# Performance work log

Measured on AMD Instinct MI355X. Metric: run time of the kernel, lower is better.

Reference implementation:

```python
import jax, jax.numpy as jnp
import numpy as np

IN_COUNT, OUT_COUNT, NUM_BASIS = 512, 512, 8
X_MIN, X_MAX, GAMMA_SCALE = 0.0, 1.0, 3.0
BATCH = 8192


def setup_inputs() -> dict:
    key = jax.random.key(0)
    k_x, k_c = jax.random.split(key)
    x = jax.random.uniform(k_x, (BATCH, IN_COUNT), dtype=jnp.float32)
    coeffs = 0.01 * jax.random.normal(k_c, (OUT_COUNT, IN_COUNT, NUM_BASIS), dtype=jnp.float32)
    centers_1d = jnp.linspace(X_MIN, X_MAX, NUM_BASIS, dtype=jnp.float32)
    centers = jnp.tile(centers_1d[None, :], (IN_COUNT, 1))  # (in, basis)
    delta = (X_MAX - X_MIN) / (NUM_BASIS - 1)
    gamma = GAMMA_SCALE / delta
    slopes = jnp.full((IN_COUNT, NUM_BASIS), gamma, dtype=jnp.float32)
    return {"x": x, "coeffs": coeffs, "centers": centers, "slopes": slopes}


def reference(x, coeffs, centers, slopes):
    # s_im(x) = 0.5 * (1 + tanh(gamma_im * (x_bi - c_im)))  -> (batch, in, basis)
    basis = 0.5 * (1.0 + jnp.tanh(slopes[None, :, :] * (x[:, :, None] - centers[None, :, :])))
    # y_bj = sum_{i,m} a_jim * s_bim : fused double reduction (GEMM-shaped)
    y = jnp.einsum('bim,jim->bj', basis, coeffs)
    return y
```

## Files before the change

kernel.cpp:

```cpp
#include <hip/hip_runtime.h>

#define BATCH 8192
#define INC   512
#define OUTC  512
#define NB    8
#define KDIM  (INC * NB)

#define BM 64
#define BN 128
#define BK 64
#define NKT (KDIM / BK)
#define LDA 72
#define THREADS 256

typedef __attribute__((ext_vector_type(8))) short bf16x8;
typedef __attribute__((ext_vector_type(4))) float f32x4;
typedef __attribute__((ext_vector_type(4))) int   i32x4;

static __device__ __forceinline__ unsigned int pk2(float lo, float hi) {
    return __builtin_amdgcn_perm(__builtin_bit_cast(unsigned int, hi),
                                 __builtin_bit_cast(unsigned int, lo),
                                 0x07060302u);
}

static __device__ __forceinline__ i32x4 pk8(float4 a, float4 b) {
    return (i32x4){(int)pk2(a.x, a.y), (int)pk2(a.z, a.w),
                   (int)pk2(b.x, b.y), (int)pk2(b.z, b.w)};
}

__global__ __launch_bounds__(256)
void w_prepass(const float* __restrict__ W, unsigned short* __restrict__ Wb) {
    const int base = (blockIdx.x * 256 + threadIdx.x) * 8;
    const float4 a = *(const float4*)(W + base);
    const float4 b = *(const float4*)(W + base + 4);
    const float v[8] = {a.x, a.y, a.z, a.w, b.x, b.y, b.z, b.w};
    unsigned int r[8];
#pragma unroll
    for (int i = 0; i < 8; ++i) {
        unsigned int t = __builtin_bit_cast(unsigned int, v[i]);
        t += 0x7FFFu + ((t >> 16) & 1u);
        r[i] = t >> 16;
    }
    i32x4 out = {(int)(r[0] | (r[1] << 16)), (int)(r[2] | (r[3] << 16)),
                 (int)(r[4] | (r[5] << 16)), (int)(r[6] | (r[7] << 16))};
    *(i32x4*)(Wb + base) = out;
}

template <bool DMA>
__global__ __launch_bounds__(THREADS, 2)
void tanh_basis_fused_gemm(const float* __restrict__ X,
                           const void*  __restrict__ Wsrc,
                           const float* __restrict__ CEN,
                           const float* __restrict__ SLP,
                           float* __restrict__ Y)
{
    __shared__ short As[BM][LDA];
    __shared__ short Bs[BN * BK];

    const int tid  = threadIdx.x;
    const int lane = tid & 63;
    const int wave = tid >> 6;
    const int wm   = wave & 1;
    const int wn   = wave >> 1;

    const int b0 = blockIdx.x * BM;
    const int j0 = blockIdx.y * BN;

    const float L2E = 1.4426950408889634f;
    const float g2  = 2.0f * SLP[0] * L2E;
    const float pc  = -g2;
    const float q0  = g2 * CEN[0];
    const float R   = __builtin_amdgcn_exp2f(g2 * (CEN[1] - CEN[0]));

    const int arow = tid >> 2;
    const int acol = (tid & 3) * 2;
    const float* xp = X + (size_t)(b0 + arow) * INC + acol;

    f32x4 acc[2][4];
#pragma unroll
    for (int i = 0; i < 2; ++i)
#pragma unroll
        for (int j = 0; j < 4; ++j)
            acc[i][j] = (f32x4){0.f, 0.f, 0.f, 0.f};

    const short* const arp = &As[wm * 32 + (lane & 15)][(lane >> 4) * 8];
    const short* const brp = &Bs[(wn * 64 + (lane & 15)) * BK + (lane >> 4) * 8];

    float2 xv = *(const float2*)xp;

    for (int kt = 0; kt < NKT; ++kt) {
        if constexpr (DMA) {
            const unsigned short* Wb = (const unsigned short*)Wsrc;
#pragma unroll
            for (int q = 0; q < 4; ++q) {
                const int cc = wave * 4 + q;
                const unsigned short* gp = Wb
                    + (size_t)(j0 + cc * 8 + (lane >> 3)) * KDIM
                    + kt * BK + (lane & 7) * 8;
                __builtin_amdgcn_global_load_lds(
                    (const __attribute__((address_space(1))) void*)gp,
                    (__attribute__((address_space(3))) void*)(Bs + cc * 512),
                    16, 0, 0);
            }
        } else {
            const float* Wf = (const float*)Wsrc;
            const int brow = tid >> 1;
            const int bkh  = tid & 1;
            const float* wp = Wf + (size_t)(j0 + brow) * KDIM + kt * BK + bkh * 32;
            float4 cv[8];
#pragma unroll
            for (int q = 0; q < 8; ++q) cv[q] = ((const float4*)wp)[q];
            i32x4* bw = (i32x4*)(Bs + brow * BK + bkh * 32);
            bw[0] = pk8(cv[0], cv[1]);
            bw[1] = pk8(cv[2], cv[3]);
            bw[2] = pk8(cv[4], cv[5]);
            bw[3] = pk8(cv[6], cv[7]);
        }

        const int ktn = (kt + 1 < NKT) ? (kt + 1) : (NKT - 1);
        const float2 xn = *(const float2*)(xp + ktn * NB);

        {
            float t0 = fmaf(pc, xv.x, q0);
            float e  = __builtin_amdgcn_exp2f(t0);
            float s[NB];
#pragma unroll
            for (int m = 0; m < NB; ++m) {
                s[m] = __builtin_amdgcn_rcpf(1.0f + e);
                e *= R;
            }
            *(i32x4*)(&As[arow][acol * 8]) =
                (i32x4){(int)pk2(s[0], s[1]), (int)pk2(s[2], s[3]),
                        (int)pk2(s[4], s[5]), (int)pk2(s[6], s[7])};

            t0 = fmaf(pc, xv.y, q0);
            e  = __builtin_amdgcn_exp2f(t0);
#pragma unroll
            for (int m = 0; m < NB; ++m) {
                s[m] = __builtin_amdgcn_rcpf(1.0f + e);
                e *= R;
            }
            *(i32x4*)(&As[arow][(acol + 1) * 8]) =
                (i32x4){(int)pk2(s[0], s[1]), (int)pk2(s[2], s[3]),
                        (int)pk2(s[4], s[5]), (int)pk2(s[6], s[7])};
        }

        __syncthreads();

#pragma unroll
        for (int ks = 0; ks < 2; ++ks) {
            bf16x8 af[2], bfr[4];
#pragma unroll
            for (int mf = 0; mf < 2; ++mf)
                af[mf] = *(const bf16x8*)(arp + mf * 16 * LDA + ks * 32);
#pragma unroll
            for (int nf = 0; nf < 4; ++nf)
                bfr[nf] = *(const bf16x8*)(brp + nf * 16 * BK + ks * 32);
#pragma unroll
            for (int mf = 0; mf < 2; ++mf)
#pragma unroll
                for (int nf = 0; nf < 4; ++nf)
                    acc[mf][nf] = __builtin_amdgcn_mfma_f32_16x16x32_bf16(
                        af[mf], bfr[nf], acc[mf][nf], 0, 0, 0);
        }

        __syncthreads();

        xv = xn;
    }

    const int lm = (lane >> 4) * 4;
    const int ln = lane & 15;
    const int rowb = b0 + wm * 32 + lm;
    const int colb = j0 + wn * 64 + ln;
#pragma unroll
    for (int mf = 0; mf < 2; ++mf)
#pragma unroll
        for (int nf = 0; nf < 4; ++nf)
#pragma unroll
            for (int r = 0; r < 4; ++r)
                Y[(size_t)(rowb + mf * 16 + r) * OUTC + (colb + nf * 16)] = acc[mf][nf][r];
}

extern "C" void kernel_launch(void* const* d_in, const int* in_sizes, int n_in,
                              void* d_out, int out_size, void* d_ws, size_t ws_size,
                              hipStream_t stream) {
    const float* X   = (const float*)d_in[0];
    const float* W   = (const float*)d_in[1];
    const float* CEN = (const float*)d_in[2];
    const float* SLP = (const float*)d_in[3];
    float* Y = (float*)d_out;

    static_assert(BATCH % BM == 0 && OUTC % BN == 0 && KDIM % BK == 0, "tiling");
    dim3 grid(BATCH / BM, OUTC / BN);

    const size_t WB_BYTES = (size_t)OUTC * KDIM * sizeof(unsigned short);
    if (ws_size >= WB_BYTES) {
        w_prepass<<<dim3((OUTC * KDIM) / (8 * 256)), dim3(256), 0, stream>>>(
            W, (unsigned short*)d_ws);
        tanh_basis_fused_gemm<true><<<grid, dim3(THREADS), 0, stream>>>(
            X, d_ws, CEN, SLP, Y);
    } else {
        tanh_basis_fused_gemm<false><<<grid, dim3(THREADS), 0, stream>>>(
            X, (const void*)W, CEN, SLP, Y);
    }
}
```

Before: 135.1 us.

## Split-K fused GEMM with register-computed basis, double-buffered swizzled B, transposed X

Restructures the fused kernel. It uses 4-way split-K with atomicAdd into a zeroed output, larger 128x128 tiles with 2 waves each holding a 64x128 accumulator, and double-buffered XOR-swizzled LDS for the bf16 weights. The tanh-basis A fragments are now built directly in registers instead of being staged through LDS. A new prepass transposes X so each lane's x loads coalesce across the batch. Together these aim to cut LDS traffic and syncs and to overlap weight staging with compute. The cost is extra prepass and memset launches, float atomics that make summation order nondeterministic, and heavy register pressure from the 32 accumulators.

```diff
diff --git a/kernel.cpp b/kernel.cpp
--- a/kernel.cpp
+++ b/kernel.cpp
@@ -5,13 +5,13 @@
 #define OUTC  512
 #define NB    8
 #define KDIM  (INC * NB)
-
-#define BM 64
-#define BN 128
-#define BK 64
-#define NKT (KDIM / BK)
-#define LDA 72
-#define THREADS 256
+#define SPLITK 4
+#define KQ    (KDIM / SPLITK)
+#define BK    64
+#define NKT   (KQ / BK)
+#define BM    128
+#define BN    128
+#define THREADS 128
 
 typedef __attribute__((ext_vector_type(8))) short bf16x8;
 typedef __attribute__((ext_vector_type(4))) float f32x4;
@@ -21,11 +21,6 @@
     return __builtin_amdgcn_perm(__builtin_bit_cast(unsigned int, hi),
                                  __builtin_bit_cast(unsigned int, lo),
                                  0x07060302u);
-}
-
-static __device__ __forceinline__ i32x4 pk8(float4 a, float4 b) {
-    return (i32x4){(int)pk2(a.x, a.y), (int)pk2(a.z, a.w),
-                   (int)pk2(b.x, b.y), (int)pk2(b.z, b.w)};
 }
 
 __global__ __launch_bounds__(256)
@@ -41,30 +36,52 @@
         t += 0x7FFFu + ((t >> 16) & 1u);
         r[i] = t >> 16;
     }
-    i32x4 out = {(int)(r[0] | (r[1] << 16)), (int)(r[2] | (r[3] << 16)),
-                 (int)(r[4] | (r[5] << 16)), (int)(r[6] | (r[7] << 16))};
-    *(i32x4*)(Wb + base) = out;
-}
-
-template <bool DMA>
+    *(i32x4*)(Wb + base) = (i32x4){(int)(r[0] | (r[1] << 16)), (int)(r[2] | (r[3] << 16)),
+                                   (int)(r[4] | (r[5] << 16)), (int)(r[6] | (r[7] << 16))};
+}
+
+__global__ __launch_bounds__(256)
+void xt_prepass(const float* __restrict__ X, float* __restrict__ XT) {
+    __shared__ float t[64][65];
+    const int bx = blockIdx.x * 64;
+    const int iy = blockIdx.y * 64;
+    const int lx = threadIdx.x & 63;
+    const int ly = threadIdx.x >> 6;
+#pragma unroll
+    for (int r = 0; r < 16; ++r) {
+        const int row = ly * 16 + r;
+        t[row][lx] = X[(size_t)(bx + row) * INC + iy + lx];
+    }
+    __syncthreads();
+#pragma unroll
+    for (int r = 0; r < 16; ++r) {
+        const int row = ly * 16 + r;
+        XT[(size_t)(iy + row) * BATCH + bx + lx] = t[lx][row];
+    }
+}
+
+template <bool DMA, bool XTP>
 __global__ __launch_bounds__(THREADS, 2)
-void tanh_basis_fused_gemm(const float* __restrict__ X,
-                           const void*  __restrict__ Wsrc,
-                           const float* __restrict__ CEN,
-                           const float* __restrict__ SLP,
-                           float* __restrict__ Y)
+void fused_gemm(const float* __restrict__ X,
+                const void*  __restrict__ Wsrc,
+                const float* __restrict__ XT,
+                const float* __restrict__ CEN,
+                const float* __restrict__ SLP,
+                float* __restrict__ Y)
 {
-    __shared__ short As[BM][LDA];
-    __shared__ short Bs[BN * BK];
+    __shared__ short Bs[2][BN * BK];
 
     const int tid  = threadIdx.x;
     const int lane = tid & 63;
     const int wave = tid >> 6;
-    const int wm   = wave & 1;
-    const int wn   = wave >> 1;
+    const int l15  = lane & 15;
+    const int h    = lane >> 4;
+    const int low3 = l15 & 7;
 
     const int b0 = blockIdx.x * BM;
     const int j0 = blockIdx.y * BN;
+    const int kz = blockIdx.z;
+    const int i00 = kz * (KQ / NB);
 
     const float L2E = 1.4426950408889634f;
     const float g2  = 2.0f * SLP[0] * L2E;
@@ -72,114 +89,126 @@
     const float q0  = g2 * CEN[0];
     const float R   = __builtin_amdgcn_exp2f(g2 * (CEN[1] - CEN[0]));
 
-    const int arow = tid >> 2;
-    const int acol = (tid & 3) * 2;
-    const float* xp = X + (size_t)(b0 + arow) * INC + acol;
-
-    f32x4 acc[2][4];
-#pragma unroll
-    for (int i = 0; i < 2; ++i)
-#pragma unroll
-        for (int j = 0; j < 4; ++j)
+    const short* const brp0 = &Bs[0][l15 * 64 + ((0 + h) ^ low3) * 8];
+    const short* const brp1 = &Bs[0][l15 * 64 + ((4 + h) ^ low3) * 8];
+
+    const int dma_r  = lane >> 3;
+    const int dma_kb = (lane & 7) ^ dma_r;
+
+    const int mrow = b0 + wave * 64 + l15;
+
+    f32x4 acc[4][8];
+#pragma unroll
+    for (int i = 0; i < 4; ++i)
+#pragma unroll
+        for (int j = 0; j < 8; ++j)
             acc[i][j] = (f32x4){0.f, 0.f, 0.f, 0.f};
 
-    const short* const arp = &As[wm * 32 + (lane & 15)][(lane >> 4) * 8];
-    const short* const brp = &Bs[(wn * 64 + (lane & 15)) * BK + (lane >> 4) * 8];
-
-    float2 xv = *(const float2*)xp;
+    float xv[8], xn[8];
+
+#define LOADX(kt, dst)                                                         \
+    {                                                                          \
+        _Pragma("unroll")                                                      \
+        for (int ks = 0; ks < 2; ++ks) {                                       \
+            const int ii = i00 + (kt) * 8 + ks * 4 + h;                        \
+            _Pragma("unroll")                                                  \
+            for (int mf = 0; mf < 4; ++mf) {                                   \
+                const int bb = mrow + mf * 16;                                 \
+                (dst)[ks * 4 + mf] = XTP ? XT[(size_t)ii * BATCH + bb]         \
+                                         : X[(size_t)bb * INC + ii];           \
+            }                                                                  \
+        }                                                                      \
+    }
+
+#define STAGEB(kt, buf)                                                        \
+    {                                                                          \
+        const int kg = kz * KQ + (kt) * BK;                                    \
+        if constexpr (DMA) {                                                   \
+            const unsigned short* Wb = (const unsigned short*)Wsrc;            \
+            _Pragma("unroll")                                                  \
+            for (int q = 0; q < 8; ++q) {                                      \
+                const int cc = wave * 8 + q;                                   \
+                const unsigned short* gp = Wb                                  \
+                    + (size_t)(j0 + cc * 8 + dma_r) * KDIM + kg + dma_kb * 8;  \
+                __builtin_amdgcn_global_load_lds(                              \
+                    (const __attribute__((address_space(1))) void*)gp,         \
+                    (__attribute__((address_space(3))) void*)(&Bs[buf][cc * 512]), \
+                    16, 0, 0);                                                 \
+            }                                                                  \
+        } else {                                                               \
+            const float* Wf = (const float*)Wsrc;                              \
+            const int row = tid;                                               \
+            const float* wp = Wf + (size_t)(j0 + row) * KDIM + kg;             \
+            _Pragma("unroll")                                                  \
+            for (int kb = 0; kb < 8; ++kb) {                                   \
+                const float4 c0 = ((const float4*)wp)[2 * kb];                 \
+                const float4 c1 = ((const float4*)wp)[2 * kb + 1];             \
+                *(i32x4*)(&Bs[buf][row * 64 + ((kb ^ (row & 7)) * 8)]) =       \
+                    (i32x4){(int)pk2(c0.x, c0.y), (int)pk2(c0.z, c0.w),        \
+                            (int)pk2(c1.x, c1.y), (int)pk2(c1.z, c1.w)};       \
+            }                                                                  \
+        }                                                                      \
+    }
+
+    LOADX(0, xv);
+    STAGEB(0, 0);
 
     for (int kt = 0; kt < NKT; ++kt) {
-        if constexpr (DMA) {
-            const unsigned short* Wb = (const unsigned short*)Wsrc;
-#pragma unroll
-            for (int q = 0; q < 4; ++q) {
-                const int cc = wave * 4 + q;
-                const unsigned short* gp = Wb
-                    + (size_t)(j0 + cc * 8 + (lane >> 3)) * KDIM
-                    + kt * BK + (lane & 7) * 8;
-                __builtin_amdgcn_global_load_lds(
-                    (const __attribute__((address_space(1))) void*)gp,
-                    (__attribute__((address_space(3))) void*)(Bs + cc * 512),
-                    16, 0, 0);
+        const int cur = kt & 1;
+
+        __syncthreads();
+
+        if (kt + 1 < NKT) STAGEB(kt + 1, 1 - cur);
+        const int ktn = (kt + 1 < NKT) ? (kt + 1) : (NKT - 1);
+        LOADX(ktn, xn);
+
+#pragma unroll
+        for (int ks = 0; ks < 2; ++ks) {
+            const short* brp = (ks ? brp1 : brp0) + cur * (BN * BK);
+            bf16x8 bfr[8];
+#pragma unroll
+            for (int nf = 0; nf < 8; ++nf)
+                bfr[nf] = *(const bf16x8*)(brp + nf * 1024);
+
+            bf16x8 af[4];
+#pragma unroll
+            for (int mf = 0; mf < 4; ++mf) {
+                float e = __builtin_amdgcn_exp2f(fmaf(pc, xv[ks * 4 + mf], q0));
+                float s[NB];
+#pragma unroll
+                for (int m = 0; m < NB; ++m) {
+                    s[m] = __builtin_amdgcn_rcpf(1.0f + e);
+                    e *= R;
+                }
+                af[mf] = __builtin_bit_cast(bf16x8,
+                    (i32x4){(int)pk2(s[0], s[1]), (int)pk2(s[2], s[3]),
+                            (int)pk2(s[4], s[5]), (int)pk2(s[6], s[7])});
             }
-        } else {
-            const float* Wf = (const float*)Wsrc;
-            const int brow = tid >> 1;
-            const int bkh  = tid & 1;
-            const float* wp = Wf + (size_t)(j0 + brow) * KDIM + kt * BK + bkh * 32;
-            float4 cv[8];
-#pragma unroll
-            for (int q = 0; q < 8; ++q) cv[q] = ((const float4*)wp)[q];
-            i32x4* bw = (i32x4*)(Bs + brow * BK + bkh * 32);
-            bw[0] = pk8(cv[0], cv[1]);
-            bw[1] = pk8(cv[2], cv[3]);
-            bw[2] = pk8(cv[4], cv[5]);
-            bw[3] = pk8(cv[6], cv[7]);
-        }
-
-        const int ktn = (kt + 1 < NKT) ? (kt + 1) : (NKT - 1);
-        const float2 xn = *(const float2*)(xp + ktn * NB);
-
-        {
-            float t0 = fmaf(pc, xv.x, q0);
-            float e  = __builtin_amdgcn_exp2f(t0);
-            float s[NB];
-#pragma unroll
-            for (int m = 0; m < NB; ++m) {
-                s[m] = __builtin_amdgcn_rcpf(1.0f + e);
-                e *= R;
-            }
-            *(i32x4*)(&As[arow][acol * 8]) =
-                (i32x4){(int)pk2(s[0], s[1]), (int)pk2(s[2], s[3]),
-                        (int)pk2(s[4], s[5]), (int)pk2(s[6], s[7])};
-
-            t0 = fmaf(pc, xv.y, q0);
-            e  = __builtin_amdgcn_exp2f(t0);
-#pragma unroll
-            for (int m = 0; m < NB; ++m) {
-                s[m] = __builtin_amdgcn_rcpf(1.0f + e);
-                e *= R;
-            }
-            *(i32x4*)(&As[arow][(acol + 1) * 8]) =
-                (i32x4){(int)pk2(s[0], s[1]), (int)pk2(s[2], s[3]),
-                        (int)pk2(s[4], s[5]), (int)pk2(s[6], s[7])};
-        }
-
-        __syncthreads();
-
-#pragma unroll
-        for (int ks = 0; ks < 2; ++ks) {
-            bf16x8 af[2], bfr[4];
-#pragma unroll
-            for (int mf = 0; mf < 2; ++mf)
-                af[mf] = *(const bf16x8*)(arp + mf * 16 * LDA + ks * 32);
-#pragma unroll
-            for (int nf = 0; nf < 4; ++nf)
-                bfr[nf] = *(const bf16x8*)(brp + nf * 16 * BK + ks * 32);
-#pragma unroll
-            for (int mf = 0; mf < 2; ++mf)
-#pragma unroll
-                for (int nf = 0; nf < 4; ++nf)
+
+#pragma unroll
+            for (int mf = 0; mf < 4; ++mf)
+#pragma unroll
+                for (int nf = 0; nf < 8; ++nf)
                     acc[mf][nf] = __builtin_amdgcn_mfma_f32_16x16x32_bf16(
                         af[mf], bfr[nf], acc[mf][nf], 0, 0, 0);
         }
 
-        __syncthreads();
-
-        xv = xn;
-    }
-
-    const int lm = (lane >> 4) * 4;
-    const int ln = lane & 15;
-    const int rowb = b0 + wm * 32 + lm;
-    const int colb = j0 + wn * 64 + ln;
-#pragma unroll
-    for (int mf = 0; mf < 2; ++mf)
-#pragma unroll
-        for (int nf = 0; nf < 4; ++nf)
+#pragma unroll
+        for (int q = 0; q < 8; ++q) xv[q] = xn[q];
+    }
+
+    const int rowb = b0 + wave * 64 + h * 4;
+    const int colb = j0 + l15;
+#pragma unroll
+    for (int mf = 0; mf < 4; ++mf)
+#pragma unroll
+        for (int nf = 0; nf < 8; ++nf)
 #pragma unroll
             for (int r = 0; r < 4; ++r)
-                Y[(size_t)(rowb + mf * 16 + r) * OUTC + (colb + nf * 16)] = acc[mf][nf][r];
+                atomicAdd(&Y[(size_t)(rowb + mf * 16 + r) * OUTC + (colb + nf * 16)],
+                          acc[mf][nf][r]);
+#undef LOADX
+#undef STAGEB
 }
 
 extern "C" void kernel_launch(void* const* d_in, const int* in_sizes, int n_in,
@@ -191,17 +220,27 @@
     const float* SLP = (const float*)d_in[3];
     float* Y = (float*)d_out;
 
-    static_assert(BATCH % BM == 0 && OUTC % BN == 0 && KDIM % BK == 0, "tiling");
-    dim3 grid(BATCH / BM, OUTC / BN);
+    hipMemsetAsync(d_out, 0, (size_t)out_size * sizeof(float), stream);
+
+    dim3 grid(BATCH / BM, OUTC / BN, SPLITK);
 
     const size_t WB_BYTES = (size_t)OUTC * KDIM * sizeof(unsigned short);
-    if (ws_size >= WB_BYTES) {
-        w_prepass<<<dim3((OUTC * KDIM) / (8 * 256)), dim3(256), 0, stream>>>(
-            W, (unsigned short*)d_ws);
-        tanh_basis_fused_gemm<true><<<grid, dim3(THREADS), 0, stream>>>(
-            X, d_ws, CEN, SLP, Y);
+    const size_t XT_BYTES = (size_t)BATCH * INC * sizeof(float);
+
+    if (ws_size >= WB_BYTES + XT_BYTES) {
+        unsigned short* Wb = (unsigned short*)d_ws;
+        float* XT = (float*)((char*)d_ws + WB_BYTES);
+        w_prepass<<<dim3((OUTC * KDIM) / (8 * 256)), dim3(256), 0, stream>>>(W, Wb);
+        xt_prepass<<<dim3(BATCH / 64, INC / 64), dim3(256), 0, stream>>>(X, XT);
+        fused_gemm<true, true><<<grid, dim3(THREADS), 0, stream>>>(
+            X, Wb, XT, CEN, SLP, Y);
+    } else if (ws_size >= WB_BYTES) {
+        unsigned short* Wb = (unsigned short*)d_ws;
+        w_prepass<<<dim3((OUTC * KDIM) / (8 * 256)), dim3(256), 0, stream>>>(W, Wb);
+        fused_gemm<true, false><<<grid, dim3(THREADS), 0, stream>>>(
+            X, Wb, nullptr, CEN, SLP, Y);
     } else {
-        tanh_basis_fused_gemm<false><<<grid, dim3(THREADS), 0, stream>>>(
-            X, (const void*)W, CEN, SLP, Y);
-    }
-}
+        fused_gemm<false, false><<<grid, dim3(THREADS), 0, stream>>>(
+            X, (const void*)W, nullptr, CEN, SLP, Y);
+    }
+}
```

After: 160.0 us. +18.4%, slower.
